# Kernel tuning notes

Hardware: AMD Instinct MI355X
Metric: run time of the kernel (lower is better)

Reference implementation:

```python
import jax, jax.numpy as jnp
import numpy as np

N = 170000          # n_users + n_entities
NNZ = 2720000       # edges in sparse A_in (avg degree 16)
DIMS = [64, 64, 32, 16]
NEG_SLOPE = 0.01    # nn.LeakyReLU default
EPS = 1e-12         # F.normalize eps


def setup_inputs() -> dict:
    key = jax.random.key(0)
    ks = jax.random.split(key, 20)
    inp = {
        "embeddings": jax.random.normal(ks[0], (N, DIMS[0]), jnp.float32) * 0.1,
        "a_vals": jax.random.uniform(ks[1], (NNZ,), jnp.float32) / 16.0,  # ~row-normalized
    }
    # bi-interaction layer params, stored (in, out) so y = x @ W + b
    i = 2
    for l in range(3):
        din, dout = DIMS[l], DIMS[l + 1]
        s = 1.0 / np.sqrt(din)
        inp[f"w1_{l}"] = jax.random.normal(ks[i], (din, dout), jnp.float32) * s; i += 1
        inp[f"b1_{l}"] = jnp.zeros((dout,), jnp.float32)
        inp[f"w2_{l}"] = jax.random.normal(ks[i], (din, dout), jnp.float32) * s; i += 1
        inp[f"b2_{l}"] = jnp.zeros((dout,), jnp.float32)
    inp["a_rows"] = jax.random.randint(ks[i], (NNZ,), 0, N, jnp.int32); i += 1
    inp["a_cols"] = jax.random.randint(ks[i], (NNZ,), 0, N, jnp.int32)
    return inp


def _leaky(x):
    return jnp.where(x >= 0, x, NEG_SLOPE * x)


def _l2norm(x):
    n = jnp.sqrt(jnp.sum(x * x, axis=1, keepdims=True))
    return x / jnp.maximum(n, EPS)


def _spmm(vals, rows, cols, emb):
    # sparse A (COO) @ emb : gather source rows, scale, scatter-add to dest rows
    msgs = vals[:, None] * emb[cols]          # (nnz, d)
    return jax.ops.segment_sum(msgs, rows, num_segments=N)


def reference(embeddings, a_vals,
              w1_0, b1_0, w2_0, b2_0,
              w1_1, b1_1, w2_1, b2_1,
              w1_2, b1_2, w2_2, b2_2,
              a_rows, a_cols):
    layers = [(w1_0, b1_0, w2_0, b2_0),
              (w1_1, b1_1, w2_1, b2_1),
              (w1_2, b1_2, w2_2, b2_2)]
    ego = embeddings
    all_embed = [ego]
    for (w1, b1, w2, b2) in layers:
        side = _spmm(a_vals, a_rows, a_cols, ego)            # (N, d_in)
        sum_e = _leaky((ego + side) @ w1 + b1)               # bi-interaction
        bi_e = _leaky((ego * side) @ w2 + b2)
        ego = sum_e + bi_e                                   # dropout = identity (eval)
        all_embed.append(_l2norm(ego))
    return jnp.concatenate(all_embed, axis=1)                # (N, 176)
```

## Files before the change

kernel.cpp:

```cpp
#include <hip/hip_runtime.h>
#include <hip/hip_bf16.h>

#define NEG_SLOPE 0.01f
#define L2EPS 1e-12f
#define SCAN_CHUNK 2048
#define PART_CH 8192
#define BSHIFT 9

__device__ __forceinline__ unsigned short f2bf(float f) {
    unsigned u = __float_as_uint(f);
    return (unsigned short)((u + 0x7fffu + ((u >> 16) & 1u)) >> 16);
}


__global__ void scan_sum(const int* __restrict__ counts, int* __restrict__ partials, int n) {
    __shared__ int red[256];
    int base = blockIdx.x * SCAN_CHUNK;
    int s = 0;
    for (int i = threadIdx.x; i < SCAN_CHUNK; i += 256) {
        int idx = base + i;
        s += (idx < n) ? counts[idx] : 0;
    }
    red[threadIdx.x] = s; __syncthreads();
    for (int o = 128; o > 0; o >>= 1) {
        if (threadIdx.x < o) red[threadIdx.x] += red[threadIdx.x + o];
        __syncthreads();
    }
    if (threadIdx.x == 0) partials[blockIdx.x] = red[0];
}

__global__ void scan_partials(int* __restrict__ partials, int nb, int* __restrict__ out, int n) {
    if (threadIdx.x == 0 && blockIdx.x == 0) {
        int run = 0;
        for (int i = 0; i < nb; i++) { int v = partials[i]; partials[i] = run; run += v; }
        out[n] = run;
    }
}

__global__ void scan_apply(const int* __restrict__ counts, const int* __restrict__ partials,
                           int* __restrict__ out, int n) {
    __shared__ int lsum[256];
    int base = blockIdx.x * SCAN_CHUNK;
    int t = threadIdx.x;
    int my[8];
    int s = 0;
    int tb = base + t * 8;
    for (int i = 0; i < 8; i++) { int idx = tb + i; int v = (idx < n) ? counts[idx] : 0; my[i] = v; s += v; }
    lsum[t] = s; __syncthreads();
    for (int o = 1; o < 256; o <<= 1) {
        int v = (t >= o) ? lsum[t - o] : 0;
        __syncthreads();
        lsum[t] += v;
        __syncthreads();
    }
    int excl = lsum[t] - s + partials[blockIdx.x];
    for (int i = 0; i < 8; i++) {
        int idx = tb + i;
        if (idx < n) { out[idx] = excl; excl += my[i]; }
    }
}


__global__ void part_hist(const int* __restrict__ rows, int* __restrict__ hist,
                          int nnz, int nchunks, int B) {
    __shared__ int h[512];
    int c = blockIdx.x;
    for (int i = threadIdx.x; i < B; i += 256) h[i] = 0;
    __syncthreads();
    int s = c * PART_CH, e = min(s + PART_CH, nnz);
    for (int i = s + threadIdx.x; i < e; i += 256) atomicAdd(&h[rows[i] >> BSHIFT], 1);
    __syncthreads();
    for (int b = threadIdx.x; b < B; b += 256) hist[b * nchunks + c] = h[b];
}

__global__ void part_scatter(const int* __restrict__ rows, const int* __restrict__ cols,
                             const float* __restrict__ vals, const int* __restrict__ hscan,
                             int2* __restrict__ tmp, int nnz, int nchunks, int B) {
    __shared__ int cur[512];
    int c = blockIdx.x;
    for (int b = threadIdx.x; b < B; b += 256) cur[b] = hscan[b * nchunks + c];
    __syncthreads();
    int s = c * PART_CH, e = min(s + PART_CH, nnz);
    for (int i = s + threadIdx.x; i < e; i += 256) {
        int r = rows[i];
        int p = atomicAdd(&cur[r >> BSHIFT], 1);
        unsigned u14 = __float2uint_rn(vals[i] * 262144.0f);
        if (u14 > 16383u) u14 = 16383u;
        tmp[p] = make_int2(((r & 511) << 18) | cols[i], (int)u14);
    }
}

__global__ void bucket_scatter(const int* __restrict__ hscan, const int2* __restrict__ tmp,
                               unsigned* __restrict__ pedge, int* __restrict__ offsets,
                               int nnz, int nchunks, int B, int n) {
    __shared__ int cnt[512];
    __shared__ int scn[256];
    int b = blockIdx.x;
    int t = threadIdx.x;
    int rbase = b << BSHIFT;
    cnt[t] = 0; cnt[t + 256] = 0;
    __syncthreads();
    int s = hscan[b * nchunks];
    int e = (b == B - 1) ? nnz : hscan[(b + 1) * nchunks];
    for (int j = s + t; j < e; j += 256) atomicAdd(&cnt[((unsigned)tmp[j].x) >> 18], 1);
    __syncthreads();
    int c0 = cnt[2 * t], c1 = cnt[2 * t + 1];
    int ssum = c0 + c1;
    scn[t] = ssum;
    __syncthreads();
    for (int o = 1; o < 256; o <<= 1) {
        int v = (t >= o) ? scn[t - o] : 0;
        __syncthreads();
        scn[t] += v;
        __syncthreads();
    }
    int excl = scn[t] - ssum + s;
    int g0 = rbase + 2 * t, g1 = g0 + 1;
    if (g0 < n) offsets[g0] = excl;
    if (g1 < n) offsets[g1] = excl + c0;
    cnt[2 * t] = excl;
    cnt[2 * t + 1] = excl + c0;
    if (b == B - 1 && t == 0) offsets[n] = nnz;
    __syncthreads();
    for (int j = s + t; j < e; j += 256) {
        int2 tt = tmp[j];
        int r9 = ((unsigned)tt.x) >> 18;
        int p = atomicAdd(&cnt[r9], 1);
        pedge[p] = (unsigned)(tt.x & 0x3FFFF) | ((unsigned)tt.y << 18);
    }
}


__global__ void embed_prep(const float* __restrict__ emb, unsigned short* __restrict__ egob,
                           unsigned char* __restrict__ qtab, float* __restrict__ scale,
                           float* __restrict__ outp, int nrows) {
    int idx = blockIdx.x * blockDim.x + threadIdx.x;
    if (idx >= nrows * 16) return;
    int row = idx >> 4, c = idx & 15;
    float4 v = ((const float4*)emb)[idx];
    ((float4*)(outp + (size_t)row * 176))[c] = v;
    ushort4 o;
    o.x = f2bf(v.x); o.y = f2bf(v.y); o.z = f2bf(v.z); o.w = f2bf(v.w);
    ((ushort4*)egob)[idx] = o;
    float mx = fmaxf(fmaxf(fabsf(v.x), fabsf(v.y)), fmaxf(fabsf(v.z), fabsf(v.w)));
#pragma unroll
    for (int s = 8; s > 0; s >>= 1) mx = fmaxf(mx, __shfl_xor(mx, s, 64));
    float qinv = mx > 0.f ? 127.f / mx : 0.f;
    int q0 = __float2int_rn(v.x * qinv);
    int q1 = __float2int_rn(v.y * qinv);
    int q2 = __float2int_rn(v.z * qinv);
    int q3 = __float2int_rn(v.w * qinv);
    unsigned w = (unsigned)(q0 & 0xff) | ((unsigned)(q1 & 0xff) << 8) |
                 ((unsigned)(q2 & 0xff) << 16) | ((unsigned)(q3 & 0xff) << 24);
    ((unsigned*)qtab)[idx] = w;
    if (c == 0) scale[row] = mx * (1.f / 127.f);
}


__device__ __forceinline__ float leaky1(float x) { return x >= 0.f ? x : NEG_SLOPE * x; }

__device__ __forceinline__ void fma4_i8(float vs, unsigned w, float* acc) {
    acc[0] += vs * (float)(char)(w & 0xffu);
    acc[1] += vs * (float)(char)((w >> 8) & 0xffu);
    acc[2] += vs * (float)(char)((w >> 16) & 0xffu);
    acc[3] += vs * (float)(char)(w >> 24);
}

__device__ __forceinline__ void unpack8(uint4 qv, float* e) {
    e[0] = __uint_as_float(qv.x << 16); e[1] = __uint_as_float(qv.x & 0xffff0000u);
    e[2] = __uint_as_float(qv.y << 16); e[3] = __uint_as_float(qv.y & 0xffff0000u);
    e[4] = __uint_as_float(qv.z << 16); e[5] = __uint_as_float(qv.z & 0xffff0000u);
    e[6] = __uint_as_float(qv.w << 16); e[7] = __uint_as_float(qv.w & 0xffff0000u);
}

#define V14 3.814697265625e-06f

template <int DIN, int DOUT>
__global__ __launch_bounds__(256, 4)
void fused_layer(const unsigned short* __restrict__ egob, const unsigned char* __restrict__ qtab,
                 const float* __restrict__ scale, const int* __restrict__ offs,
                 const unsigned* __restrict__ pedge,
                 const float* __restrict__ w1, const float* __restrict__ b1,
                 const float* __restrict__ w2, const float* __restrict__ b2,
                 unsigned short* __restrict__ egob_next, unsigned char* __restrict__ qtab_next,
                 float* __restrict__ scale_next,
                 float* __restrict__ outp, int col_off, int nrows) {
    constexpr int RPB = 64;
    constexpr int CPL = DIN / 4;
    constexpr int U4  = CPL / 8;
    constexpr int W   = CPL / 4;
    constexpr int TX  = DOUT / 4;
    constexpr int TY  = 256 / TX;
    constexpr int RPT = RPB / TY;

    __shared__ float sU[DIN][RPB];
    __shared__ float sV[DIN][RPB];

    int tid = threadIdx.x;
    int row0 = blockIdx.x * RPB;

    if (tid < 64) {
        int g = row0 + tid;
        unsigned deg = (g < nrows) ? (unsigned)(offs[g + 1] - offs[g]) : 0u;
        unsigned key = (deg << 6) | (unsigned)tid;
#pragma unroll
        for (int size = 2; size <= 64; size <<= 1) {
#pragma unroll
            for (int stride = size >> 1; stride > 0; stride >>= 1) {
                unsigned other = __shfl_xor(key, stride, 64);
                bool dir = ((tid & size) == 0);
                bool lower = ((tid & stride) == 0);
                bool takeMin = (lower == dir);
                key = takeMin ? (key < other ? key : other) : (key > other ? key : other);
            }
        }
        ((int*)sU)[tid] = (int)(key & 63u);
    }
    __syncthreads();
    int r = tid >> 2, q = tid & 3;
    int pr = ((int*)sU)[r];
    __syncthreads();

    {
        int g = row0 + pr;
        float acc[CPL];
#pragma unroll
        for (int i = 0; i < CPL; i++) acc[i] = 0.f;
        if (g < nrows) {
            int j0 = offs[g], j1 = offs[g + 1];
            uint4 eq[U4];
            const uint4* ep = (const uint4*)(egob + (size_t)g * DIN) + q * U4;
#pragma unroll
            for (int u = 0; u < U4; u++) eq[u] = ep[u];

            int j = j0;
            unsigned ed[4];
            bool have = (j + 4 <= j1);
            if (have) {
#pragma unroll
                for (int m = 0; m < 4; m++) ed[m] = pedge[j + m];
            }
            while (have) {
                unsigned tw[4][W];
                float scv[4];
#pragma unroll
                for (int m = 0; m < 4; m++) {
                    unsigned col = ed[m] & 0x3FFFFu;
                    const unsigned* qp = (const unsigned*)(qtab + (size_t)col * DIN) + q * W;
                    if constexpr (W == 4) {
                        uint4 v4 = *(const uint4*)qp;
                        tw[m][0] = v4.x; tw[m][1] = v4.y; tw[m][2] = v4.z; tw[m][3] = v4.w;
                    } else {
                        uint2 v2 = *(const uint2*)qp;
                        tw[m][0] = v2.x; tw[m][1] = v2.y;
                    }
                    scv[m] = scale[col];
                }
                bool nxt = (j + 8 <= j1);
                unsigned ed2[4];
                if (nxt) {
#pragma unroll
                    for (int m = 0; m < 4; m++) ed2[m] = pedge[j + 4 + m];
                }
#pragma unroll
                for (int m = 0; m < 4; m++) {
                    float vs = (float)(ed[m] >> 18) * V14 * scv[m];
#pragma unroll
                    for (int w = 0; w < W; w++) fma4_i8(vs, tw[m][w], acc + w * 4);
                }
#pragma unroll
                for (int m = 0; m < 4; m++) ed[m] = ed2[m];
                j += 4;
                have = nxt;
            }
            for (; j < j1; ++j) {
                unsigned e0 = pedge[j];
                unsigned col = e0 & 0x3FFFFu;
                const unsigned* qp = (const unsigned*)(qtab + (size_t)col * DIN) + q * W;
                unsigned tw0[W];
                if constexpr (W == 4) {
                    uint4 v4 = *(const uint4*)qp;
                    tw0[0] = v4.x; tw0[1] = v4.y; tw0[2] = v4.z; tw0[3] = v4.w;
                } else {
                    uint2 v2 = *(const uint2*)qp;
                    tw0[0] = v2.x; tw0[1] = v2.y;
                }
                float vs = (float)(e0 >> 18) * V14 * scale[col];
#pragma unroll
                for (int w = 0; w < W; w++) fma4_i8(vs, tw0[w], acc + w * 4);
            }
#pragma unroll
            for (int u = 0; u < U4; u++) {
                float ev[8];
                unpack8(eq[u], ev);
                int k0 = q * CPL + u * 8;
#pragma unroll
                for (int z = 0; z < 8; z++) {
                    float e = ev[z], a = acc[u * 8 + z];
                    sU[k0 + z][pr] = e + a;
                    sV[k0 + z][pr] = e * a;
                }
            }
        } else {
#pragma unroll
            for (int i = 0; i < CPL; i++) { sU[q * CPL + i][pr] = 0.f; sV[q * CPL + i][pr] = 0.f; }
        }
    }
    __syncthreads();

    int tx = tid % TX, ty = tid / TX;
    float4 a1[RPT], a2[RPT];
#pragma unroll
    for (int i = 0; i < RPT; i++) {
        a1[i] = make_float4(0.f, 0.f, 0.f, 0.f);
        a2[i] = make_float4(0.f, 0.f, 0.f, 0.f);
    }

#pragma unroll 8
    for (int k = 0; k < DIN; k++) {
        float4 w1v = ((const float4*)w1)[k * TX + tx];
        float4 w2v = ((const float4*)w2)[k * TX + tx];
        float uv[RPT], vv[RPT];
        if constexpr (RPT == 4) {
            float4 t1 = *(const float4*)&sU[k][ty * 4];
            float4 t2 = *(const float4*)&sV[k][ty * 4];
            uv[0] = t1.x; uv[1] = t1.y; uv[2] = t1.z; uv[3] = t1.w;
            vv[0] = t2.x; vv[1] = t2.y; vv[2] = t2.z; vv[3] = t2.w;
        } else if constexpr (RPT == 2) {
            float2 t1 = *(const float2*)&sU[k][ty * 2];
            float2 t2 = *(const float2*)&sV[k][ty * 2];
            uv[0] = t1.x; uv[1] = t1.y;
            vv[0] = t2.x; vv[1] = t2.y;
        } else {
            uv[0] = sU[k][ty];
            vv[0] = sV[k][ty];
        }
#pragma unroll
        for (int i = 0; i < RPT; i++) {
            a1[i].x += uv[i] * w1v.x; a1[i].y += uv[i] * w1v.y; a1[i].z += uv[i] * w1v.z; a1[i].w += uv[i] * w1v.w;
            a2[i].x += vv[i] * w2v.x; a2[i].y += vv[i] * w2v.y; a2[i].z += vv[i] * w2v.z; a2[i].w += vv[i] * w2v.w;
        }
    }

    float4 bb1 = ((const float4*)b1)[tx];
    float4 bb2 = ((const float4*)b2)[tx];
#pragma unroll
    for (int i = 0; i < RPT; i++) {
        int g = row0 + ty * RPT + i;
        float4 x;
        x.x = leaky1(a1[i].x + bb1.x) + leaky1(a2[i].x + bb2.x);
        x.y = leaky1(a1[i].y + bb1.y) + leaky1(a2[i].y + bb2.y);
        x.z = leaky1(a1[i].z + bb1.z) + leaky1(a2[i].z + bb2.z);
        x.w = leaky1(a1[i].w + bb1.w) + leaky1(a2[i].w + bb2.w);
        float ss = x.x * x.x + x.y * x.y + x.z * x.z + x.w * x.w;
        float mx = fmaxf(fmaxf(fabsf(x.x), fabsf(x.y)), fmaxf(fabsf(x.z), fabsf(x.w)));
#pragma unroll
        for (int o = TX >> 1; o > 0; o >>= 1) {
            ss += __shfl_xor(ss, o, 64);
            mx = fmaxf(mx, __shfl_xor(mx, o, 64));
        }
        if (g < nrows) {
            if (egob_next) {
                ushort4 xb;
                xb.x = f2bf(x.x); xb.y = f2bf(x.y); xb.z = f2bf(x.z); xb.w = f2bf(x.w);
                ((ushort4*)(egob_next + (size_t)g * DOUT))[tx] = xb;
                float qinv = mx > 0.f ? 127.f / mx : 0.f;
                int q0 = __float2int_rn(x.x * qinv);
                int q1 = __float2int_rn(x.y * qinv);
                int q2 = __float2int_rn(x.z * qinv);
                int q3 = __float2int_rn(x.w * qinv);
                unsigned wq = (unsigned)(q0 & 0xff) | ((unsigned)(q1 & 0xff) << 8) |
                              ((unsigned)(q2 & 0xff) << 16) | ((unsigned)(q3 & 0xff) << 24);
                ((unsigned*)(qtab_next + (size_t)g * DOUT))[tx] = wq;
                if (tx == 0) scale_next[g] = mx * (1.f / 127.f);
            }
            float inv = 1.f / fmaxf(sqrtf(ss), L2EPS);
            float4 y = make_float4(x.x * inv, x.y * inv, x.z * inv, x.w * inv);
            ((float4*)(outp + (size_t)g * 176 + col_off))[tx] = y;
        }
    }
}

extern "C" void kernel_launch(void* const* d_in, const int* in_sizes, int n_in,
                              void* d_out, int out_size, void* d_ws, size_t ws_size,
                              hipStream_t stream) {
    const float* emb   = (const float*)d_in[0];
    const float* avals = (const float*)d_in[1];
    const float* w1_0 = (const float*)d_in[2];  const float* b1_0 = (const float*)d_in[3];
    const float* w2_0 = (const float*)d_in[4];  const float* b2_0 = (const float*)d_in[5];
    const float* w1_1 = (const float*)d_in[6];  const float* b1_1 = (const float*)d_in[7];
    const float* w2_1 = (const float*)d_in[8];  const float* b2_1 = (const float*)d_in[9];
    const float* w1_2 = (const float*)d_in[10]; const float* b1_2 = (const float*)d_in[11];
    const float* w2_2 = (const float*)d_in[12]; const float* b2_2 = (const float*)d_in[13];
    const int* arows = (const int*)d_in[14];
    const int* acols = (const int*)d_in[15];
    float* outp = (float*)d_out;

    const int N   = in_sizes[0] / 64;
    const int NNZ = in_sizes[14];

    const int B       = (N + 511) >> BSHIFT;
    const int nchunks = (NNZ + PART_CH - 1) / PART_CH;
    const int NH      = B * nchunks;

    char* w = (char*)d_ws;
    size_t off = 0;
    auto carve = [&](size_t bytes) { char* p = w + off; off += (bytes + 255) & ~(size_t)255; return p; };
    int*   offsets  = (int*)  carve((size_t)(N + 1) * 4);
    int*   partials = (int*)  carve(1024);
    int*   hist     = (int*)  carve((size_t)(NH + 1) * 4);
    int*   hscan    = (int*)  carve((size_t)(NH + 1) * 4);
    unsigned* pedge = (unsigned*)carve((size_t)NNZ * 4);
    int2*  tmp      = (int2*) carve((size_t)NNZ * 8);
    unsigned short* egobA = (unsigned short*)carve((size_t)N * 64 * 2);
    unsigned short* egobB = (unsigned short*)carve((size_t)N * 64 * 2);
    unsigned char*  qtabA = (unsigned char*)carve((size_t)N * 64);
    unsigned char*  qtabB = (unsigned char*)carve((size_t)N * 64);
    float* scaleA   = (float*)carve((size_t)N * 4);
    float* scaleB   = (float*)carve((size_t)N * 4);

    const int NB2 = (NH + SCAN_CHUNK - 1) / SCAN_CHUNK;

    part_hist<<<nchunks, 256, 0, stream>>>(arows, hist, NNZ, nchunks, B);
    scan_sum<<<NB2, 256, 0, stream>>>(hist, partials, NH);
    scan_partials<<<1, 64, 0, stream>>>(partials, NB2, hscan, NH);
    scan_apply<<<NB2, 256, 0, stream>>>(hist, partials, hscan, NH);
    part_scatter<<<nchunks, 256, 0, stream>>>(arows, acols, avals, hscan, tmp, NNZ, nchunks, B);
    bucket_scatter<<<B, 256, 0, stream>>>(hscan, tmp, pedge, offsets, NNZ, nchunks, B, N);

    embed_prep<<<(N * 16 + 255) / 256, 256, 0, stream>>>(emb, egobA, qtabA, scaleA, outp, N);

    const int DB = (N + 63) / 64;

    fused_layer<64, 64><<<DB, 256, 0, stream>>>(egobA, qtabA, scaleA, offsets, pedge,
                                                w1_0, b1_0, w2_0, b2_0,
                                                egobB, qtabB, scaleB, outp, 64, N);
    fused_layer<64, 32><<<DB, 256, 0, stream>>>(egobB, qtabB, scaleB, offsets, pedge,
                                                w1_1, b1_1, w2_1, b2_1,
                                                egobA, qtabA, scaleA, outp, 128, N);
    fused_layer<32, 16><<<DB, 256, 0, stream>>>(egobA, qtabA, scaleA, offsets, pedge,
                                                w1_2, b1_2, w2_2, b2_2,
                                                nullptr, nullptr, nullptr, outp, 160, N);
}
```

Measured before the change: 584.1 us.

## Slice edges by source-column range and run layers as cooperative persistent grids

```diff
diff --git a/kernel.cpp b/kernel.cpp
--- a/kernel.cpp
+++ b/kernel.cpp
@@ -1,11 +1,17 @@
 #include <hip/hip_runtime.h>
 #include <hip/hip_bf16.h>
+#include <hip/hip_cooperative_groups.h>
+
+namespace cg = cooperative_groups;
 
 #define NEG_SLOPE 0.01f
 #define L2EPS 1e-12f
 #define SCAN_CHUNK 2048
 #define PART_CH 8192
 #define BSHIFT 9
+#define NSLICE 3
+#define FGRID 1024
+#define MAXT 3
 
 __device__ __forceinline__ unsigned short f2bf(float f) {
     unsigned u = __float_as_uint(f);
@@ -91,21 +97,29 @@
 }
 
 __global__ void bucket_scatter(const int* __restrict__ hscan, const int2* __restrict__ tmp,
-                               unsigned* __restrict__ pedge, int* __restrict__ offsets,
-                               int nnz, int nchunks, int B, int n) {
-    __shared__ int cnt[512];
+                               unsigned* __restrict__ pedge, int* __restrict__ offs2,
+                               int nnz, int nchunks, int B, int n, int sb1, int sb2) {
+    __shared__ int cnt[2048];
     __shared__ int scn[256];
     int b = blockIdx.x;
     int t = threadIdx.x;
     int rbase = b << BSHIFT;
-    cnt[t] = 0; cnt[t + 256] = 0;
+    for (int i = t; i < 2048; i += 256) cnt[i] = 0;
     __syncthreads();
     int s = hscan[b * nchunks];
     int e = (b == B - 1) ? nnz : hscan[(b + 1) * nchunks];
-    for (int j = s + t; j < e; j += 256) atomicAdd(&cnt[((unsigned)tmp[j].x) >> 18], 1);
-    __syncthreads();
-    int c0 = cnt[2 * t], c1 = cnt[2 * t + 1];
-    int ssum = c0 + c1;
+    for (int j = s + t; j < e; j += 256) {
+        unsigned x = (unsigned)tmp[j].x;
+        int col = (int)(x & 0x3FFFFu);
+        int sl = (col >= sb2) ? 2 : ((col >= sb1) ? 1 : 0);
+        atomicAdd(&cnt[(int)((x >> 18) << 2) | sl], 1);
+    }
+    __syncthreads();
+    int base = t * 8;
+    int vals[8];
+    int ssum = 0;
+#pragma unroll
+    for (int i = 0; i < 8; i++) { vals[i] = cnt[base + i]; ssum += vals[i]; }
     scn[t] = ssum;
     __syncthreads();
     for (int o = 1; o < 256; o <<= 1) {
@@ -115,18 +129,27 @@
         __syncthreads();
     }
     int excl = scn[t] - ssum + s;
-    int g0 = rbase + 2 * t, g1 = g0 + 1;
-    if (g0 < n) offsets[g0] = excl;
-    if (g1 < n) offsets[g1] = excl + c0;
-    cnt[2 * t] = excl;
-    cnt[2 * t + 1] = excl + c0;
-    if (b == B - 1 && t == 0) offsets[n] = nnz;
+#pragma unroll
+    for (int i = 0; i < 8; i++) { cnt[base + i] = excl; excl += vals[i]; }
+    __syncthreads();
+    {
+        int r0 = 2 * t;
+#pragma unroll
+        for (int rr = 0; rr < 2; rr++) {
+            int rl = r0 + rr;
+            int g = rbase + rl;
+#pragma unroll
+            for (int sl = 0; sl < 4; sl++) offs2[g * 4 + sl] = cnt[(rl << 2) | sl];
+        }
+    }
     __syncthreads();
     for (int j = s + t; j < e; j += 256) {
         int2 tt = tmp[j];
-        int r9 = ((unsigned)tt.x) >> 18;
-        int p = atomicAdd(&cnt[r9], 1);
-        pedge[p] = (unsigned)(tt.x & 0x3FFFF) | ((unsigned)tt.y << 18);
+        unsigned x = (unsigned)tt.x;
+        int col = (int)(x & 0x3FFFFu);
+        int sl = (col >= sb2) ? 2 : ((col >= sb1) ? 1 : 0);
+        int p = atomicAdd(&cnt[(int)((x >> 18) << 2) | sl], 1);
+        pedge[p] = (x & 0x3FFFFu) | ((unsigned)tt.y << 18);
     }
 }
 
@@ -175,65 +198,75 @@
 
 #define V14 3.814697265625e-06f
 
-template <int DIN, int DOUT>
+template <int DIN, int DOUT, bool COOP>
 __global__ __launch_bounds__(256, 4)
 void fused_layer(const unsigned short* __restrict__ egob, const unsigned char* __restrict__ qtab,
-                 const float* __restrict__ scale, const int* __restrict__ offs,
+                 const float* __restrict__ scale, const int* __restrict__ offs2,
                  const unsigned* __restrict__ pedge,
                  const float* __restrict__ w1, const float* __restrict__ b1,
                  const float* __restrict__ w2, const float* __restrict__ b2,
                  unsigned short* __restrict__ egob_next, unsigned char* __restrict__ qtab_next,
                  float* __restrict__ scale_next,
                  float* __restrict__ outp, int col_off, int nrows) {
-    constexpr int RPB = 64;
     constexpr int CPL = DIN / 4;
     constexpr int U4  = CPL / 8;
     constexpr int W   = CPL / 4;
     constexpr int TX  = DOUT / 4;
     constexpr int TY  = 256 / TX;
-    constexpr int RPT = RPB / TY;
-
-    __shared__ float sU[DIN][RPB];
-    __shared__ float sV[DIN][RPB];
+    constexpr int RPT = 64 / TY;
+
+    __shared__ float sU[DIN][64];
+    __shared__ float sV[DIN][64];
+    __shared__ int   perm[MAXT][64];
 
     int tid = threadIdx.x;
-    int row0 = blockIdx.x * RPB;
+    int bid = blockIdx.x;
 
     if (tid < 64) {
-        int g = row0 + tid;
-        unsigned deg = (g < nrows) ? (unsigned)(offs[g + 1] - offs[g]) : 0u;
-        unsigned key = (deg << 6) | (unsigned)tid;
-#pragma unroll
-        for (int size = 2; size <= 64; size <<= 1) {
-#pragma unroll
-            for (int stride = size >> 1; stride > 0; stride >>= 1) {
-                unsigned other = __shfl_xor(key, stride, 64);
-                bool dir = ((tid & size) == 0);
-                bool lower = ((tid & stride) == 0);
-                bool takeMin = (lower == dir);
-                key = takeMin ? (key < other ? key : other) : (key > other ? key : other);
-            }
-        }
-        ((int*)sU)[tid] = (int)(key & 63u);
+        for (int tt = 0; tt < MAXT; tt++) {
+            int row0 = (bid + tt * FGRID) * 64;
+            int g = row0 + tid;
+            unsigned deg = (row0 < nrows && g < nrows)
+                         ? (unsigned)(offs2[g * 4 + 3] - offs2[g * 4]) : 0u;
+            unsigned key = (deg << 6) | (unsigned)tid;
+#pragma unroll
+            for (int size = 2; size <= 64; size <<= 1) {
+#pragma unroll
+                for (int stride = size >> 1; stride > 0; stride >>= 1) {
+                    unsigned other = __shfl_xor(key, stride, 64);
+                    bool dir = ((tid & size) == 0);
+                    bool lower = ((tid & stride) == 0);
+                    bool takeMin = (lower == dir);
+                    key = takeMin ? (key < other ? key : other) : (key > other ? key : other);
+                }
+            }
+            perm[tt][tid] = (int)(key & 63u);
+        }
     }
     __syncthreads();
     int r = tid >> 2, q = tid & 3;
-    int pr = ((int*)sU)[r];
-    __syncthreads();
-
-    {
-        int g = row0 + pr;
-        float acc[CPL];
-#pragma unroll
-        for (int i = 0; i < CPL; i++) acc[i] = 0.f;
-        if (g < nrows) {
-            int j0 = offs[g], j1 = offs[g + 1];
-            uint4 eq[U4];
-            const uint4* ep = (const uint4*)(egob + (size_t)g * DIN) + q * U4;
-#pragma unroll
-            for (int u = 0; u < U4; u++) eq[u] = ep[u];
-
-            int j = j0;
+    int gt[MAXT];
+    bool vt[MAXT];
+#pragma unroll
+    for (int tt = 0; tt < MAXT; tt++) {
+        int row0 = (bid + tt * FGRID) * 64;
+        vt[tt] = (row0 < nrows);
+        gt[tt] = row0 + perm[tt][r];
+    }
+
+    float acc[MAXT][CPL];
+#pragma unroll
+    for (int tt = 0; tt < MAXT; tt++)
+#pragma unroll
+        for (int i = 0; i < CPL; i++) acc[tt][i] = 0.f;
+
+    for (int s = 0; s < NSLICE; s++) {
+#pragma unroll
+        for (int tt = 0; tt < MAXT; tt++) {
+            if (!vt[tt]) continue;
+            int g = gt[tt];
+            if (g >= nrows) continue;
+            int j = offs2[g * 4 + s], j1 = offs2[g * 4 + s + 1];
             unsigned ed[4];
             bool have = (j + 4 <= j1);
             if (have) {
@@ -266,7 +299,7 @@
                 for (int m = 0; m < 4; m++) {
                     float vs = (float)(ed[m] >> 18) * V14 * scv[m];
 #pragma unroll
-                    for (int w = 0; w < W; w++) fma4_i8(vs, tw[m][w], acc + w * 4);
+                    for (int w = 0; w < W; w++) fma4_i8(vs, tw[m][w], acc[tt] + w * 4);
                 }
 #pragma unroll
                 for (int m = 0; m < 4; m++) ed[m] = ed2[m];
@@ -287,8 +320,23 @@
                 }
                 float vs = (float)(e0 >> 18) * V14 * scale[col];
 #pragma unroll
-                for (int w = 0; w < W; w++) fma4_i8(vs, tw0[w], acc + w * 4);
-            }
+                for (int w = 0; w < W; w++) fma4_i8(vs, tw0[w], acc[tt] + w * 4);
+            }
+        }
+        if (COOP && s < NSLICE - 1) cg::this_grid().sync();
+    }
+
+#pragma unroll
+    for (int tt = 0; tt < MAXT; tt++) {
+        if (!vt[tt]) break;
+        int row0 = (bid + tt * FGRID) * 64;
+        int g = gt[tt];
+        int pr = g - row0;
+        if (g < nrows) {
+            uint4 eq[U4];
+            const uint4* ep = (const uint4*)(egob + (size_t)g * DIN) + q * U4;
+#pragma unroll
+            for (int u = 0; u < U4; u++) eq[u] = ep[u];
 #pragma unroll
             for (int u = 0; u < U4; u++) {
                 float ev[8];
@@ -296,7 +344,7 @@
                 int k0 = q * CPL + u * 8;
 #pragma unroll
                 for (int z = 0; z < 8; z++) {
-                    float e = ev[z], a = acc[u * 8 + z];
+                    float e = ev[z], a = acc[tt][u * 8 + z];
                     sU[k0 + z][pr] = e + a;
                     sV[k0 + z][pr] = e * a;
                 }
@@ -305,79 +353,101 @@
 #pragma unroll
             for (int i = 0; i < CPL; i++) { sU[q * CPL + i][pr] = 0.f; sV[q * CPL + i][pr] = 0.f; }
         }
-    }
-    __syncthreads();
-
-    int tx = tid % TX, ty = tid / TX;
-    float4 a1[RPT], a2[RPT];
-#pragma unroll
-    for (int i = 0; i < RPT; i++) {
-        a1[i] = make_float4(0.f, 0.f, 0.f, 0.f);
-        a2[i] = make_float4(0.f, 0.f, 0.f, 0.f);
-    }
+        __syncthreads();
+
+        int tx = tid % TX, ty = tid / TX;
+        float4 a1[RPT], a2[RPT];
+#pragma unroll
+        for (int i = 0; i < RPT; i++) {
+            a1[i] = make_float4(0.f, 0.f, 0.f, 0.f);
+            a2[i] = make_float4(0.f, 0.f, 0.f, 0.f);
+        }
 
 #pragma unroll 8
-    for (int k = 0; k < DIN; k++) {
-        float4 w1v = ((const float4*)w1)[k * TX + tx];
-        float4 w2v = ((const float4*)w2)[k * TX + tx];
-        float uv[RPT], vv[RPT];
-        if constexpr (RPT == 4) {
-            float4 t1 = *(const float4*)&sU[k][ty * 4];
-            float4 t2 = *(const float4*)&sV[k][ty * 4];
-            uv[0] = t1.x; uv[1] = t1.y; uv[2] = t1.z; uv[3] = t1.w;
-            vv[0] = t2.x; vv[1] = t2.y; vv[2] = t2.z; vv[3] = t2.w;
-        } else if constexpr (RPT == 2) {
-            float2 t1 = *(const float2*)&sU[k][ty * 2];
-            float2 t2 = *(const float2*)&sV[k][ty * 2];
-            uv[0] = t1.x; uv[1] = t1.y;
-            vv[0] = t2.x; vv[1] = t2.y;
-        } else {
-            uv[0] = sU[k][ty];
-            vv[0] = sV[k][ty];
-        }
+        for (int k = 0; k < DIN; k++) {
+            float4 w1v = ((const float4*)w1)[k * TX + tx];
+            float4 w2v = ((const float4*)w2)[k * TX + tx];
+            float uv[RPT], vv[RPT];
+            if constexpr (RPT == 4) {
+                float4 t1 = *(const float4*)&sU[k][ty * 4];
+                float4 t2 = *(const float4*)&sV[k][ty * 4];
+                uv[0] = t1.x; uv[1] = t1.y; uv[2] = t1.z; uv[3] = t1.w;
+                vv[0] = t2.x; vv[1] = t2.y; vv[2] = t2.z; vv[3] = t2.w;
+            } else if constexpr (RPT == 2) {
+                float2 t1 = *(const float2*)&sU[k][ty * 2];
+                float2 t2 = *(const float2*)&sV[k][ty * 2];
+                uv[0] = t1.x; uv[1] = t1.y;
+                vv[0] = t2.x; vv[1] = t2.y;
+            } else {
+                uv[0] = sU[k][ty];
+                vv[0] = sV[k][ty];
+            }
+#pragma unroll
+            for (int i = 0; i < RPT; i++) {
+                a1[i].x += uv[i] * w1v.x; a1[i].y += uv[i] * w1v.y; a1[i].z += uv[i] * w1v.z; a1[i].w += uv[i] * w1v.w;
+                a2[i].x += vv[i] * w2v.x; a2[i].y += vv[i] * w2v.y; a2[i].z += vv[i] * w2v.z; a2[i].w += vv[i] * w2v.w;
+            }
+        }
+
+        float4 bb1 = ((const float4*)b1)[tx];
+        float4 bb2 = ((const float4*)b2)[tx];
 #pragma unroll
         for (int i = 0; i < RPT; i++) {
-            a1[i].x += uv[i] * w1v.x; a1[i].y += uv[i] * w1v.y; a1[i].z += uv[i] * w1v.z; a1[i].w += uv[i] * w1v.w;
-            a2[i].x += vv[i] * w2v.x; a2[i].y += vv[i] * w2v.y; a2[i].z += vv[i] * w2v.z; a2[i].w += vv[i] * w2v.w;
-        }
-    }
-
-    float4 bb1 = ((const float4*)b1)[tx];
-    float4 bb2 = ((const float4*)b2)[tx];
-#pragma unroll
-    for (int i = 0; i < RPT; i++) {
-        int g = row0 + ty * RPT + i;
-        float4 x;
-        x.x = leaky1(a1[i].x + bb1.x) + leaky1(a2[i].x + bb2.x);
-        x.y = leaky1(a1[i].y + bb1.y) + leaky1(a2[i].y + bb2.y);
-        x.z = leaky1(a1[i].z + bb1.z) + leaky1(a2[i].z + bb2.z);
-        x.w = leaky1(a1[i].w + bb1.w) + leaky1(a2[i].w + bb2.w);
-        float ss = x.x * x.x + x.y * x.y + x.z * x.z + x.w * x.w;
-        float mx = fmaxf(fmaxf(fabsf(x.x), fabsf(x.y)), fmaxf(fabsf(x.z), fabsf(x.w)));
-#pragma unroll
-        for (int o = TX >> 1; o > 0; o >>= 1) {
-            ss += __shfl_xor(ss, o, 64);
-            mx = fmaxf(mx, __shfl_xor(mx, o, 64));
-        }
-        if (g < nrows) {
-            if (egob_next) {
-                ushort4 xb;
-                xb.x = f2bf(x.x); xb.y = f2bf(x.y); xb.z = f2bf(x.z); xb.w = f2bf(x.w);
-                ((ushort4*)(egob_next + (size_t)g * DOUT))[tx] = xb;
-                float qinv = mx > 0.f ? 127.f / mx : 0.f;
-                int q0 = __float2int_rn(x.x * qinv);
-                int q1 = __float2int_rn(x.y * qinv);
-                int q2 = __float2int_rn(x.z * qinv);
-                int q3 = __float2int_rn(x.w * qinv);
-                unsigned wq = (unsigned)(q0 & 0xff) | ((unsigned)(q1 & 0xff) << 8) |
-                              ((unsigned)(q2 & 0xff) << 16) | ((unsigned)(q3 & 0xff) << 24);
-                ((unsigned*)(qtab_next + (size_t)g * DOUT))[tx] = wq;
-                if (tx == 0) scale_next[g] = mx * (1.f / 127.f);
-            }
-            float inv = 1.f / fmaxf(sqrtf(ss), L2EPS);
-            float4 y = make_float4(x.x * inv, x.y * inv, x.z * inv, x.w * inv);
-            ((float4*)(outp + (size_t)g * 176 + col_off))[tx] = y;
-        }
+            int go = row0 + ty * RPT + i;
+            float4 x;
+            x.x = leaky1(a1[i].x + bb1.x) + leaky1(a2[i].x + bb2.x);
+            x.y = leaky1(a1[i].y + bb1.y) + leaky1(a2[i].y + bb2.y);
+            x.z = leaky1(a1[i].z + bb1.z) + leaky1(a2[i].z + bb2.z);
+            x.w = leaky1(a1[i].w + bb1.w) + leaky1(a2[i].w + bb2.w);
+            float ss = x.x * x.x + x.y * x.y + x.z * x.z + x.w * x.w;
+            float mx = fmaxf(fmaxf(fabsf(x.x), fabsf(x.y)), fmaxf(fabsf(x.z), fabsf(x.w)));
+#pragma unroll
+            for (int o = TX >> 1; o > 0; o >>= 1) {
+                ss += __shfl_xor(ss, o, 64);
+                mx = fmaxf(mx, __shfl_xor(mx, o, 64));
+            }
+            if (go < nrows) {
+                if (egob_next) {
+                    ushort4 xb;
+                    xb.x = f2bf(x.x); xb.y = f2bf(x.y); xb.z = f2bf(x.z); xb.w = f2bf(x.w);
+                    ((ushort4*)(egob_next + (size_t)go * DOUT))[tx] = xb;
+                    float qinv = mx > 0.f ? 127.f / mx : 0.f;
+                    int q0 = __float2int_rn(x.x * qinv);
+                    int q1 = __float2int_rn(x.y * qinv);
+                    int q2 = __float2int_rn(x.z * qinv);
+                    int q3 = __float2int_rn(x.w * qinv);
+                    unsigned wq = (unsigned)(q0 & 0xff) | ((unsigned)(q1 & 0xff) << 8) |
+                                  ((unsigned)(q2 & 0xff) << 16) | ((unsigned)(q3 & 0xff) << 24);
+                    ((unsigned*)(qtab_next + (size_t)go * DOUT))[tx] = wq;
+                    if (tx == 0) scale_next[go] = mx * (1.f / 127.f);
+                }
+                float inv = 1.f / fmaxf(sqrtf(ss), L2EPS);
+                float4 y = make_float4(x.x * inv, x.y * inv, x.z * inv, x.w * inv);
+                ((float4*)(outp + (size_t)go * 176 + col_off))[tx] = y;
+            }
+        }
+        __syncthreads();
+    }
+}
+
+template <int DIN, int DOUT>
+static void launch_fused(const unsigned short* egob, const unsigned char* qtab,
+                         const float* scale, const int* offs2, const unsigned* pedge,
+                         const float* w1, const float* b1, const float* w2, const float* b2,
+                         unsigned short* egob_next, unsigned char* qtab_next, float* scale_next,
+                         float* outp, int col_off, int nrows, hipStream_t stream) {
+    void* args[] = {(void*)&egob, (void*)&qtab, (void*)&scale, (void*)&offs2, (void*)&pedge,
+                    (void*)&w1, (void*)&b1, (void*)&w2, (void*)&b2,
+                    (void*)&egob_next, (void*)&qtab_next, (void*)&scale_next,
+                    (void*)&outp, (void*)&col_off, (void*)&nrows};
+    hipError_t err = hipLaunchCooperativeKernel(
+        reinterpret_cast<void*>(&fused_layer<DIN, DOUT, true>),
+        dim3(FGRID), dim3(256), args, 0, stream);
+    if (err != hipSuccess) {
+        (void)hipGetLastError();
+        fused_layer<DIN, DOUT, false><<<FGRID, 256, 0, stream>>>(
+            egob, qtab, scale, offs2, pedge, w1, b1, w2, b2,
+            egob_next, qtab_next, scale_next, outp, col_off, nrows);
     }
 }
 
@@ -402,11 +472,13 @@
     const int B       = (N + 511) >> BSHIFT;
     const int nchunks = (NNZ + PART_CH - 1) / PART_CH;
     const int NH      = B * nchunks;
+    const int sb1     = (N + NSLICE - 1) / NSLICE;
+    const int sb2     = 2 * sb1;
 
     char* w = (char*)d_ws;
     size_t off = 0;
     auto carve = [&](size_t bytes) { char* p = w + off; off += (bytes + 255) & ~(size_t)255; return p; };
-    int*   offsets  = (int*)  carve((size_t)(N + 1) * 4);
+    int*   offs2    = (int*)  carve((size_t)B * 512 * 4 * 4);
     int*   partials = (int*)  carve(1024);
     int*   hist     = (int*)  carve((size_t)(NH + 1) * 4);
     int*   hscan    = (int*)  carve((size_t)(NH + 1) * 4);
@@ -426,19 +498,14 @@
     scan_partials<<<1, 64, 0, stream>>>(partials, NB2, hscan, NH);
     scan_apply<<<NB2, 256, 0, stream>>>(hist, partials, hscan, NH);
     part_scatter<<<nchunks, 256, 0, stream>>>(arows, acols, avals, hscan, tmp, NNZ, nchunks, B);
-    bucket_scatter<<<B, 256, 0, stream>>>(hscan, tmp, pedge, offsets, NNZ, nchunks, B, N);
+    bucket_scatter<<<B, 256, 0, stream>>>(hscan, tmp, pedge, offs2, NNZ, nchunks, B, N, sb1, sb2);
 
     embed_prep<<<(N * 16 + 255) / 256, 256, 0, stream>>>(emb, egobA, qtabA, scaleA, outp, N);
 
-    const int DB = (N + 63) / 64;
-
-    fused_layer<64, 64><<<DB, 256, 0, stream>>>(egobA, qtabA, scaleA, offsets, pedge,
-                                                w1_0, b1_0, w2_0, b2_0,
-                                                egobB, qtabB, scaleB, outp, 64, N);
-    fused_layer<64, 32><<<DB, 256, 0, stream>>>(egobB, qtabB, scaleB, offsets, pedge,
-                                                w1_1, b1_1, w2_1, b2_1,
-                                                egobA, qtabA, scaleA, outp, 128, N);
-    fused_layer<32, 16><<<DB, 256, 0, stream>>>(egobA, qtabA, scaleA, offsets, pedge,
-                                                w1_2, b1_2, w2_2, b2_2,
-                                                nullptr, nullptr, nullptr, outp, 160, N);
-}
+    launch_fused<64, 64>(egobA, qtabA, scaleA, offs2, pedge, w1_0, b1_0, w2_0, b2_0,
+                         egobB, qtabB, scaleB, outp, 64, N, stream);
+    launch_fused<64, 32>(egobB, qtabB, scaleB, offs2, pedge, w1_1, b1_1, w2_1, b2_1,
+                         egobA, qtabA, scaleA, outp, 128, N, stream);
+    launch_fused<32, 16>(egobA, qtabA, scaleA, offs2, pedge, w1_2, b1_2, w2_2, b2_2,
+                         nullptr, nullptr, nullptr, outp, 160, N, stream);
+}
```

New measurement: 1.525 ms. 161% more time.
